# Performance work log

Hardware: AMD Instinct MI355X
Metric: run time of the kernel (lower is better)

The kernel has to match this reference:

```python
import jax, jax.numpy as jnp
import numpy as np

B, F_IN, GRID, D, C = 32768, 64, 8, 16, 10
N = GRID * GRID          # 64 nodes
HID = N * D              # 1024
ATOMS = 2
LN_EPS = 1e-5
EPS = 1e-8


def _layernorm(h):
    mu = h.mean(-1, keepdims=True)
    var = h.var(-1, keepdims=True)
    return (h - mu) / jnp.sqrt(var + LN_EPS)


def _regulator(sig, w1, b1, g, be, w2, b2):
    # Linear -> LayerNorm -> Tanh -> Linear -> Sigmoid
    h = jnp.tanh(_layernorm(sig @ w1.T + b1) * g + be)
    return jax.nn.sigmoid(h @ w2.T + b2)


def _reg_params(key, in_dim):
    k = jax.random.split(key, 4)
    return (jax.random.normal(k[0], (16, in_dim)) * 0.3,
            jax.random.normal(k[1], (16,)) * 0.1,
            jnp.ones((16,)), jnp.zeros((16,)),
            jax.random.normal(k[2], (3, 16)) * 0.3,
            jax.random.normal(k[3], (3,)) * 0.1)


def setup_inputs() -> dict:
    key = jax.random.key(0)
    ks = jax.random.split(key, 16)
    # 2D grid 4-neighbour adjacency mask (constant)
    mask = np.zeros((N, N), np.float32)
    for i in range(N):
        r, c = divmod(i, GRID)
        if r > 0: mask[i, i - GRID] = 1
        if r < GRID - 1: mask[i, i + GRID] = 1
        if c > 0: mask[i, i - 1] = 1
        if c < GRID - 1: mask[i, i + 1] = 1
    pr = _reg_params(ks[10], 3)
    cr = _reg_params(ks[11], 3)
    sr = _reg_params(ks[12], 3)
    scr = _reg_params(ks[13], 2)
    inp = {
        "x": jax.random.normal(ks[0], (B, F_IN)),
        "W_embed": jax.random.normal(ks[1], (HID, F_IN)) * 0.1,
        "b_embed": jnp.zeros((HID,)),
        "adj_weights": jax.random.normal(ks[2], (N, N)) * 0.1,
        "adj_mask": jnp.asarray(mask),
        "V_slow": jax.random.normal(ks[3], (D, D)) * 0.1,
        "W_slow": jax.random.normal(ks[4], (D, D)) * 0.1,
        "gate_w": jax.random.normal(ks[5], (1, D)) * 0.3,
        "gate_b": jnp.zeros((1,)),
        "W_fast": jax.random.normal(ks[6], (D, D)) * 0.05,  # buffer, eval mode (no Hebbian update)
        "basis": jax.random.normal(ks[7], (ATOMS, D)) * 0.5,
        "Wq": jax.random.normal(ks[8], (D, D)) * 0.2,
        "sc_w1": jax.random.normal(ks[9], (8, HID)) * 0.05,
        "sc_w2": jax.random.normal(ks[14], (4, 8)) * 0.3,
        "W_read": jax.random.normal(ks[15], (C, HID)) * 0.05,
        "b_read": jnp.zeros((C,)),
    }
    for pre, p in (("pr", pr), ("cr", cr), ("sr", sr), ("scr", scr)):
        for nm, v in zip(("w1", "b1", "g", "be", "w2", "b2"), p):
            inp[pre + "_" + nm] = v
    return inp


def reference(x, W_embed, b_embed, adj_weights, adj_mask,
              pr_w1, pr_b1, pr_g, pr_be, pr_w2, pr_b2,
              V_slow, W_slow, gate_w, gate_b, W_fast,
              cr_w1, cr_b1, cr_g, cr_be, cr_w2, cr_b2,
              basis, Wq,
              sr_w1, sr_b1, sr_g, sr_be, sr_w2, sr_b2,
              sc_w1, sc_w2,
              scr_w1, scr_b1, scr_g, scr_be, scr_w2, scr_b2,
              W_read, b_read):
    Bx = x.shape[0]
    x_embed = (x @ W_embed.T + b_embed).reshape(Bx, N, D)

    # --- AutoregulatedPlasticity adjacency ---
    sig = jnp.stack([jnp.var(x, ddof=1), jnp.abs(x_embed).mean(),
                     jnp.linalg.norm(adj_weights)])[None]
    pl = _regulator(sig, pr_w1, pr_b1, pr_g, pr_be, pr_w2, pr_b2)[0]
    adj = jax.nn.sigmoid(adj_weights * pl[0]) * adj_mask
    adj = adj / jnp.clip(adj.sum(1, keepdims=True), 1e-6, None)
    x_agg = jnp.einsum('nm,bmd->bnd', adj, x_embed)

    # --- AutoregulatedContinuum (eval: W_fast fixed) ---
    xf = x_agg.reshape(-1, D)           # [B*N, D]
    v = xf @ V_slow.T
    sig = jnp.stack([jnp.var(xf, ddof=1), jnp.abs(v).mean(),
                     jnp.linalg.norm(W_slow)])[None]
    ctrl = _regulator(sig, cr_w1, cr_b1, cr_g, cr_be, cr_w2, cr_b2)[0]
    gate = jax.nn.sigmoid(v @ gate_w.T + gate_b) * ctrl[0]   # [B*N, 1]
    fast_out = xf @ W_fast.T
    x_proc = (gate * (v + fast_out * ctrl[2])).reshape(Bx, N, D)

    # --- AutoregulatedSymbiotic, applied per node (vmapped over node axis) ---
    ortho = jnp.linalg.norm(basis @ basis.T - jnp.eye(ATOMS))
    scale = D ** 0.5 + EPS

    def sym_one(xn):  # xn: [B, D]
        w = jax.nn.softmax((xn @ Wq.T) @ basis.T / scale, axis=-1)  # [B, ATOMS]
        ent = -(w * jnp.log(w + EPS)).sum(-1).mean()
        sig_n = jnp.stack([jnp.var(xn, ddof=1), ent, ortho])[None]
        infl = _regulator(sig_n, sr_w1, sr_b1, sr_g, sr_be, sr_w2, sr_b2)[0, 0]
        return (1.0 - infl) * xn + infl * (w @ basis), ent

    refined, ents = jax.vmap(sym_one)(x_proc.transpose(1, 0, 2))  # [N,B,D]
    x_proc = refined.transpose(1, 0, 2)
    entropy = ents[-1]  # torch loop keeps the last node's entropy

    x_flat = x_proc.reshape(Bx, HID)
    logits = x_flat @ W_read.T + b_read

    # --- AutoregulatedSupConHead (entropy.item() -> detached scalar) ---
    sigc = jnp.stack([jnp.var(x_flat, ddof=1),
                      jax.lax.stop_gradient(entropy)])[None]
    gain = _regulator(sigc, scr_w1, scr_b1, scr_g, scr_be, scr_w2, scr_b2)[0, 0]
    proj = (jax.nn.relu(x_flat @ sc_w1.T) @ sc_w2.T) * gain
    return logits, proj, entropy, ortho
```

## Files before the change

kernel.cpp:

```cpp
#include <hip/hip_runtime.h>

typedef unsigned short u16;
typedef unsigned long long u64;
typedef __attribute__((ext_vector_type(8))) short short8;
typedef __attribute__((ext_vector_type(4))) float f32x4;

#define MFMA16(a,b,c) __builtin_amdgcn_mfma_f32_16x16x32_bf16(a,b,c,0,0,0)

#define B_SZ   32768
#define NNODE  64
#define NB_PAIR (B_SZ*NNODE)
#define OUT_PROJ   327680
#define OUT_ENT    458752
#define OUT_ORTHO  458753

#define OFF_SCAL   ((size_t)0)
#define OFF_ADJ    ((size_t)512)
#define OFF_BEFF   (OFF_ADJ  + 8192u)
#define OFF_WEFF   (OFF_BEFF + 4096u)
#define OFF_WCAT   (OFF_WEFF + 131072u)
#define OFF_S1     (OFF_WCAT + 65536u)
#define OFF_S2     (OFF_S1   + 12288u)
#define OFF_S3     (OFF_S2   + 12288u)
#define OFF_S4     (OFF_S3   + 2048u*192u*4u)
#define OFF_H      (OFF_S4   + 8192u)
#define OFF_W01    (OFF_H    + (size_t)B_SZ*8u*4u)
#define OFF_CAN    (OFF_W01  + (size_t)NB_PAIR*4u)

#define CAN_X      0u
#define CAN_WEMB   2097152u
#define CAN_WREAD  (CAN_WEMB + 65536u)
#define CAN_SCW1   (CAN_WREAD + 10240u)
#define CAN_SMALL  (CAN_SCW1 + 8192u)
#define CAN_TOTAL  (CAN_SMALL + 11008u)
#define OFF_BEX    (((OFF_CAN + (size_t)CAN_TOTAL*2u) + 63u) & ~(size_t)63u)
#define OFF_WET    (OFF_BEX + 48u*16u*2u)
#define OFF_VW     (OFF_WET + 131072u)
#define OFF_VB     (OFF_VW  + 131072u)
#define OFF_WC     (OFF_VB  + 4096u)
#define OFF_SW     (OFF_WC  + 131072u)
#define OFF_BC2    (OFF_SW  + 24576u)
#define OFF_SB     (OFF_BC2 + 4096u)
#define OFF_DR     (OFF_SB  + 1024u)
#define WS_NEEDED  (OFF_DR  + 192u*8u)

__device__ __forceinline__ float bf2f(u16 u){
    unsigned v = ((unsigned)u) << 16;
    return __builtin_bit_cast(float, v);
}
__device__ __forceinline__ u16 f2bf(float f){
    unsigned u = __builtin_bit_cast(unsigned, f);
    u += 0x7FFFu + ((u >> 16) & 1u);
    return (u16)(u >> 16);
}
__device__ __forceinline__ float sigm(float x){ return 1.f/(1.f + expf(-x)); }
__device__ __forceinline__ u16 conv_one(const void* src, int i, int isfp32){
    return isfp32 ? f2bf(((const float*)src)[i]) : ((const u16*)src)[i];
}
__device__ __forceinline__ void store_out(void* dout, int idx, float v, int isfp32){
    if (isfp32) ((float*)dout)[idx] = v;
    else        ((u16*)dout)[idx]   = f2bf(v);
}
__device__ __forceinline__ double blk_red(double v, double* sred, int tid){
    #pragma unroll
    for (int off = 32; off > 0; off >>= 1) v += __shfl_xor(v, off);
    if ((tid & 63) == 0) sred[tid >> 6] = v;
    __syncthreads();
    double r = sred[0] + sred[1] + sred[2] + sred[3];
    __syncthreads();
    return r;
}

__device__ void run_regulator(const u16* w1, const u16* b1, const u16* g,
                              const u16* be, const u16* w2, const u16* b2,
                              const float* sig, int in_dim, float* out)
{
    float h[16];
    float mu = 0.f;
    for (int i = 0; i < 16; ++i){
        float a = bf2f(b1[i]);
        for (int j = 0; j < in_dim; ++j) a += sig[j]*bf2f(w1[i*in_dim + j]);
        h[i] = a; mu += a;
    }
    mu *= 0.0625f;
    float var = 0.f;
    for (int i = 0; i < 16; ++i){ float d = h[i]-mu; var += d*d; }
    var *= 0.0625f;
    float inv = 1.f / sqrtf(var + 1e-5f);
    for (int i = 0; i < 16; ++i){
        float hn = (h[i]-mu)*inv;
        h[i] = tanhf(hn*bf2f(g[i]) + bf2f(be[i]));
    }
    for (int c = 0; c < 3; ++c){
        float o = bf2f(b2[c]);
        for (int i = 0; i < 16; ++i) o += h[i]*bf2f(w2[c*16 + i]);
        out[c] = sigm(o);
    }
}

__device__ __forceinline__ int probe_isfp32(const u16* xraw, int tid, int* sred)
{
    int c = 0;
    #pragma unroll
    for (int j = 0; j < 4; ++j){
        u16 u = xraw[(tid*4 + j)*2];
        int e = (u >> 7) & 0xFF;
        if (u == 0 || (e >= 90 && e <= 140)) c++;
    }
    #pragma unroll
    for (int off = 32; off > 0; off >>= 1) c += __shfl_xor(c, off);
    if ((tid & 63) == 0) sred[tid >> 6] = c;
    __syncthreads();
    int tot = sred[0]+sred[1]+sred[2]+sred[3];
    __syncthreads();
    return tot < 614;
}

__global__ __launch_bounds__(256) void kc_big(const void* x, const void* wemb,
    const void* wread, const void* scw1, u16* can, float* scal)
{
    __shared__ int sred[4];
    int tid = threadIdx.x;
    int isfp32 = probe_isfp32((const u16*)x, tid, sred);
    if (blockIdx.x == 0 && tid == 0) scal[127] = isfp32 ? 1.0f : 0.0f;
    int gid = blockIdx.x*256 + tid, stride = gridDim.x*256;
    for (int i = gid; i < 2097152; i += stride) can[CAN_X + i]     = conv_one(x, i, isfp32);
    for (int i = gid; i < 65536;   i += stride) can[CAN_WEMB + i]  = conv_one(wemb, i, isfp32);
    for (int i = gid; i < 10240;   i += stride) can[CAN_WREAD + i] = conv_one(wread, i, isfp32);
    for (int i = gid; i < 8192;    i += stride) can[CAN_SCW1 + i]  = conv_one(scw1, i, isfp32);
}

struct SmallTab { const void* src[36]; int cnt[36]; int off[36]; };
__global__ __launch_bounds__(256) void kc_small(SmallTab t, u16* can, const float* scal)
{
    int isfp32 = scal[127] != 0.f;
    int gid = blockIdx.x*256 + threadIdx.x, stride = gridDim.x*256;
    for (int e = 0; e < 36; ++e){
        const void* s = t.src[e];
        u16* d = can + t.off[e];
        int n = t.cnt[e];
        for (int i = gid; i < n; i += stride) d[i] = conv_one(s, i, isfp32);
    }
}

__global__ __launch_bounds__(256) void k0_wcat(const u16* wread, const u16* scw1,
    const u16* wemb, const u16* vslow, const u16* gatew, u16* wcat, u16* wembT, u16* bex)
{
    int b = blockIdx.x, tid = threadIdx.x;
    if (b < 128){
        int idx = b*256 + tid;
        int row = idx >> 10, k = idx & 1023;
        u16 v = 0;
        if (row < 10)      v = wread[row*1024 + k];
        else if (row < 18) v = scw1[(row-10)*1024 + k];
        wcat[idx] = v;
    } else if (b < 384){
        int idx = (b-128)*256 + tid;
        int m = idx >> 10, jj = idx & 1023;
        wembT[jj*64 + m] = wemb[m*1024 + jj];
    } else {
        if (tid < 16){
            float a = 0.f;
            for (int i = 0; i < 16; ++i) a += bf2f(gatew[i])*bf2f(vslow[i*16+tid]);
            bex[32*16+tid] = f2bf(a);
        }
    }
}

__global__ __launch_bounds__(256) void k1_embed(const u16* x, const u16* wemb,
                                                const u16* bemb, float* s1)
{
    __shared__ float red[12];
    int tid = threadIdx.x, wave = tid>>6, lane = tid&63;
    int m = lane&15, quad = lane>>4;
    int cg = blockIdx.x & 31, rc = blockIdx.x >> 5;
    int col0 = cg*32 + m, col1 = col0 + 16;
    short8 b00 = *(const short8*)(wemb + col0*64 + quad*8);
    short8 b01 = *(const short8*)(wemb + col0*64 + quad*8 + 32);
    short8 b10 = *(const short8*)(wemb + col1*64 + quad*8);
    short8 b11 = *(const short8*)(wemb + col1*64 + quad*8 + 32);
    float bias0 = bf2f(bemb[col0]), bias1 = bf2f(bemb[col1]);
    float sx = 0.f, sxx = 0.f, sabs = 0.f;
    const u16* xbase = x + (size_t)(rc*1024 + wave*256 + m)*64 + quad*8;
    #pragma unroll 4
    for (int it = 0; it < 16; ++it){
        const u16* xr = xbase + (size_t)it*16*64;
        short8 a0 = *(const short8*)xr;
        short8 a1 = *(const short8*)(xr + 32);
        if (cg == 0){
            #pragma unroll
            for (int j = 0; j < 8; ++j){
                float f0 = bf2f((u16)a0[j]); sx += f0; sxx += f0*f0;
                float f1 = bf2f((u16)a1[j]); sx += f1; sxx += f1*f1;
            }
        }
        f32x4 zc = {0.f,0.f,0.f,0.f};
        f32x4 c0 = MFMA16(a0, b00, zc);
        c0 = MFMA16(a1, b01, c0);
        f32x4 c1 = MFMA16(a0, b10, zc);
        c1 = MFMA16(a1, b11, c1);
        #pragma unroll
        for (int r = 0; r < 4; ++r)
            sabs += fabsf(c0[r]+bias0) + fabsf(c1[r]+bias1);
    }
    #pragma unroll
    for (int off = 32; off > 0; off >>= 1){
        sx   += __shfl_xor(sx, off);
        sxx  += __shfl_xor(sxx, off);
        sabs += __shfl_xor(sabs, off);
    }
    if (lane == 0){ red[wave*3] = sx; red[wave*3+1] = sxx; red[wave*3+2] = sabs; }
    __syncthreads();
    if (tid == 0){
        for (int k = 0; k < 3; ++k)
            s1[blockIdx.x*3 + k] = red[k] + red[3+k] + red[6+k] + red[9+k];
    }
}

__global__ __launch_bounds__(256) void k2_adj(const u16* adjw, const u16* adjm, const u16* bemb,
    const u16* w1, const u16* b1, const u16* g, const u16* be, const u16* w2, const u16* b2,
    const float* s1, float* scal, u16* adjb, float* beff)
{
    __shared__ double sred[4];
    __shared__ float raw[4096];
    __shared__ float rowsum[64];
    __shared__ float bembs[1024];
    __shared__ float pl0s;
    int tid = threadIdx.x;
    for (int i = tid; i < 1024; i += 256) bembs[i] = bf2f(bemb[i]);
    double s=0, ss=0, sa=0;
    for (int i = tid; i < 1024; i += 256){
        s += (double)s1[i*3]; ss += (double)s1[i*3+1]; sa += (double)s1[i*3+2];
    }
    double nq = 0;
    for (int i = tid; i < 4096; i += 256){ float f = bf2f(adjw[i]); nq += (double)(f*f); }
    double S  = blk_red(s,  sred, tid);
    double SS = blk_red(ss, sred, tid);
    double SA = blk_red(sa, sred, tid);
    double NQ = blk_red(nq, sred, tid);
    if (tid == 0){
        double nx = 2097152.0;
        float sg[3];
        sg[0] = (float)((SS - S*S/nx)/(nx - 1.0));
        sg[1] = (float)(SA / 33554432.0);
        sg[2] = sqrtf((float)NQ);
        float o[3];
        run_regulator(w1,b1,g,be,w2,b2, sg, 3, o);
        scal[0] = o[0]; pl0s = o[0];
    }
    __syncthreads();
    float pl0 = pl0s;
    for (int i = tid; i < 4096; i += 256)
        raw[i] = sigm(bf2f(adjw[i])*pl0) * bf2f(adjm[i]);
    __syncthreads();
    if (tid < 64){
        float r = 0.f;
        for (int mc = 0; mc < 64; ++mc) r += raw[tid*64 + mc];
        rowsum[tid] = fmaxf(r, 1e-6f);
    }
    __syncthreads();
    for (int i = tid; i < 4096; i += 256) adjb[i] = f2bf(raw[i] / rowsum[i>>6]);
    for (int o = tid; o < 1024; o += 256){
        int n = o >> 4, d = o & 15;
        float a = 0.f;
        for (int m = 0; m < 64; ++m) a += raw[n*64+m]*bembs[m*16+d];
        beff[o] = a / rowsum[n];
    }
}

__global__ __launch_bounds__(256) void k2b_mfma(const u16* adjb, const u16* wembT, u16* weff)
{
    int tid = threadIdx.x, wave = tid>>6, lane = tid&63;
    int m = lane&15, quad = lane>>4;
    const u16* ar = adjb + (wave*16 + m)*64 + quad*8;
    short8 a0 = *(const short8*)ar;
    short8 a1 = *(const short8*)(ar + 32);
    int col = blockIdx.x*16 + m;
    const u16* br = wembT + col*64 + quad*8;
    short8 b0 = *(const short8*)br;
    short8 b1 = *(const short8*)(br + 32);
    f32x4 acc = {0.f,0.f,0.f,0.f};
    acc = MFMA16(a0, b0, acc);
    acc = MFMA16(a1, b1, acc);
    #pragma unroll
    for (int r = 0; r < 4; ++r)
        weff[(size_t)(wave*16 + quad*4 + r)*1024 + blockIdx.x*16 + m] = f2bf(acc[r]);
}

__global__ __launch_bounds__(256) void kvw(const u16* vslow, const u16* weff, const float* beff,
                                           u16* vw, float* vbias)
{
    __shared__ float Vs[256];
    int tid = threadIdx.x, b = blockIdx.x;
    Vs[tid] = bf2f(vslow[tid]);
    __syncthreads();
    if (b < 256){
        int idx = b*256 + tid;
        int j = idx >> 6, kf = idx & 63;
        int n = j >> 4, i = j & 15;
        float a = 0.f;
        #pragma unroll
        for (int d = 0; d < 16; ++d) a += Vs[i*16+d]*bf2f(weff[(size_t)(n*16+d)*64 + kf]);
        vw[(size_t)j*64 + kf] = f2bf(a);
    } else {
        int o = (b-256)*256 + tid;
        int n = o >> 4, i = o & 15;
        float a = 0.f;
        #pragma unroll
        for (int d = 0; d < 16; ++d) a += Vs[i*16+d]*beff[n*16+d];
        vbias[o] = a;
    }
}

__global__ __launch_bounds__(256) void k3_stats(const u16* x, const u16* weff, const float* beff,
                                                const u16* vw, const float* vbias, float* s2)
{
    __shared__ float red[12];
    int tid = threadIdx.x, wave = tid>>6, lane = tid&63;
    int m = lane&15, quad = lane>>4;
    int cg = blockIdx.x & 31, rc = blockIdx.x >> 5;
    int col0 = cg*32 + m, col1 = col0 + 16;
    short8 b00 = *(const short8*)(weff + (size_t)col0*64 + quad*8);
    short8 b01 = *(const short8*)(weff + (size_t)col0*64 + quad*8 + 32);
    short8 b10 = *(const short8*)(weff + (size_t)col1*64 + quad*8);
    short8 b11 = *(const short8*)(weff + (size_t)col1*64 + quad*8 + 32);
    short8 v00 = *(const short8*)(vw + (size_t)col0*64 + quad*8);
    short8 v01 = *(const short8*)(vw + (size_t)col0*64 + quad*8 + 32);
    short8 v10 = *(const short8*)(vw + (size_t)col1*64 + quad*8);
    short8 v11 = *(const short8*)(vw + (size_t)col1*64 + quad*8 + 32);
    float be0 = beff[col0], be1 = beff[col1];
    float vb0 = vbias[col0], vb1 = vbias[col1];
    float psum=0.f, pssq=0.f, pabsv=0.f;
    const u16* xbase = x + (size_t)(rc*1024 + wave*256 + m)*64 + quad*8;
    #pragma unroll 4
    for (int it = 0; it < 16; ++it){
        const u16* xr = xbase + (size_t)it*16*64;
        short8 a0 = *(const short8*)xr;
        short8 a1 = *(const short8*)(xr + 32);
        f32x4 zc = {0.f,0.f,0.f,0.f};
        f32x4 c0 = MFMA16(a0, b00, zc);
        c0 = MFMA16(a1, b01, c0);
        f32x4 c1 = MFMA16(a0, b10, zc);
        c1 = MFMA16(a1, b11, c1);
        f32x4 w0 = MFMA16(a0, v00, zc);
        w0 = MFMA16(a1, v01, w0);
        f32x4 w1 = MFMA16(a0, v10, zc);
        w1 = MFMA16(a1, v11, w1);
        #pragma unroll
        for (int r = 0; r < 4; ++r){
            float f0 = c0[r] + be0, f1 = c1[r] + be1;
            psum += f0 + f1; pssq += f0*f0 + f1*f1;
            pabsv += fabsf(w0[r] + vb0) + fabsf(w1[r] + vb1);
        }
    }
    #pragma unroll
    for (int off = 32; off > 0; off >>= 1){
        psum  += __shfl_xor(psum, off);
        pssq  += __shfl_xor(pssq, off);
        pabsv += __shfl_xor(pabsv, off);
    }
    if (lane == 0){ red[wave*3] = psum; red[wave*3+1] = pssq; red[wave*3+2] = pabsv; }
    __syncthreads();
    if (tid == 0){
        for (int k = 0; k < 3; ++k)
            s2[blockIdx.x*3 + k] = red[k] + red[3+k] + red[6+k] + red[9+k];
    }
}

__global__ __launch_bounds__(256) void k3b_ctrl(const u16* wslow,
    const u16* vslow, const u16* wfast, const u16* wq, const u16* basis,
    const u16* w1, const u16* b1, const u16* g, const u16* be, const u16* w2, const u16* b2,
    const float* s2, float* scal, u16* bex)
{
    __shared__ double sred[4];
    __shared__ float ctrl2s;
    int tid = threadIdx.x;
    double s=0, ss=0, sv=0;
    for (int i = tid; i < 1024; i += 256){
        s += (double)s2[i*3]; ss += (double)s2[i*3+1]; sv += (double)s2[i*3+2];
    }
    float wf = bf2f(wslow[tid]);
    double nq = (double)(wf*wf);
    double S  = blk_red(s,  sred, tid);
    double SS = blk_red(ss, sred, tid);
    double SV = blk_red(sv, sred, tid);
    double NQ = blk_red(nq, sred, tid);
    if (tid == 0){
        double M = 33554432.0;
        float sg[3];
        sg[0] = (float)((SS - S*S/M)/(M - 1.0));
        sg[1] = (float)(SV / M);
        sg[2] = sqrtf((float)NQ);
        float o[3];
        run_regulator(w1,b1,g,be,w2,b2, sg, 3, o);
        scal[1] = o[0]; scal[2] = o[2];
        ctrl2s = o[2];
    }
    __syncthreads();
    float ctrl2 = ctrl2s;
    if (tid < 64){
        #pragma unroll
        for (int j = 0; j < 4; ++j){
            int idx = tid*4 + j;
            int d = idx >> 4, k = idx & 15;
            bex[(16+d)*16+k] = f2bf(bf2f(vslow[idx]) + ctrl2*bf2f(wfast[idx]));
        }
    } else if (tid < 96){
        int a = (tid-64) >> 4, k = (tid-64) & 15;
        float e = 0.f;
        for (int d = 0; d < 16; ++d){
            float bq = 0.f;
            for (int j = 0; j < 16; ++j) bq += bf2f(basis[a*16+j])*bf2f(wq[j*16+d]);
            e += bq*(bf2f(vslow[d*16+k]) + ctrl2*bf2f(wfast[d*16+k]));
        }
        bex[(33+a)*16+k] = f2bf(0.25f*e);
    }
}

__global__ __launch_bounds__(256) void kbw(const u16* bex, const u16* weff, const float* beff,
                                           const u16* gateb, u16* wc, u16* sw,
                                           float* bc, float* sb)
{
    __shared__ float BcL[256], gvL[16], e0L[16], e1L[16];
    int tid = threadIdx.x;
    if (tid < 256) BcL[tid] = bf2f(bex[(16 + (tid>>4))*16 + (tid&15)]);
    if (tid < 16){
        gvL[tid] = bf2f(bex[32*16+tid]);
        e0L[tid] = bf2f(bex[33*16+tid]);
        e1L[tid] = bf2f(bex[34*16+tid]);
    }
    __syncthreads();
    int id = blockIdx.x*256 + tid;
    if (id < 65536){
        int col = id >> 6, k = id & 63;
        int n = col >> 4, d = col & 15;
        float a = 0.f;
        #pragma unroll
        for (int dd = 0; dd < 16; ++dd)
            a += BcL[d*16+dd]*bf2f(weff[(size_t)(n*16+dd)*64 + k]);
        wc[(size_t)col*64 + k] = f2bf(a);
    } else if (id < 77824){
        int j2 = id - 65536;
        int scol = j2 >> 6, k = j2 & 63;
        int n = scol/3, j = scol - n*3;
        const float* sr = (j==0) ? gvL : (j==1) ? e0L : e1L;
        float a = 0.f;
        #pragma unroll
        for (int dd = 0; dd < 16; ++dd)
            a += sr[dd]*bf2f(weff[(size_t)(n*16+dd)*64 + k]);
        sw[(size_t)scol*64 + k] = f2bf(a);
    } else if (id < 78848){
        int col = id - 77824;
        int n = col >> 4, d = col & 15;
        float a = 0.f;
        #pragma unroll
        for (int dd = 0; dd < 16; ++dd) a += BcL[d*16+dd]*beff[n*16+dd];
        bc[col] = a;
    } else if (id < 79040){
        int s = id - 78848;
        int n = s/3, j = s - n*3;
        const float* sr = (j==0) ? gvL : (j==1) ? e0L : e1L;
        float a = 0.f;
        #pragma unroll
        for (int dd = 0; dd < 16; ++dd) a += sr[dd]*beff[n*16+dd];
        if (j == 0) a += bf2f(gateb[0]);
        sb[s] = a;
    }
}

#define SCP 193
__global__ __launch_bounds__(256) void k4_stats(const u16* x, const u16* wc, const u16* sw,
    const float* bc, const float* sb, const float* scal, unsigned* wpack, float* s3)
{
    __shared__ float sc[16*SCP];
    __shared__ float gt[1024];
    __shared__ float entp[256];
    __shared__ float snode[128];
    int tid = threadIdx.x, wave = tid>>6, lane = tid&63;
    int m = lane&15, quad = lane>>4;
    int row0 = blockIdx.x*16;
    const u16* xr = x + (row0 + m)*64 + quad*8;
    short8 a0 = *(const short8*)xr;
    short8 a1 = *(const short8*)(xr + 32);
    float ctrl0 = scal[1];
    #pragma unroll
    for (int tt = 0; tt < 3; ++tt){
        int ct = wave*3 + tt;
        int scol = ct*16 + m;
        const u16* br = sw + (size_t)scol*64 + quad*8;
        short8 b0 = *(const short8*)br;
        short8 b1 = *(const short8*)(br + 32);
        f32x4 zc = {0.f,0.f,0.f,0.f};
        f32x4 c = MFMA16(a0, b0, zc);
        c = MFMA16(a1, b1, c);
        float sbv = sb[scol];
        #pragma unroll
        for (int r = 0; r < 4; ++r)
            sc[(quad*4+r)*SCP + scol] = c[r] + sbv;
    }
    __syncthreads();
    {
        int n = tid & 63, rgrp = tid >> 6;
        float ent = 0.f;
        #pragma unroll
        for (int rr = 0; rr < 4; ++rr){
            int row = rgrp*4 + rr;
            float gd  = sc[row*SCP + 3*n];
            float e0d = sc[row*SCP + 3*n + 1];
            float e1d = sc[row*SCP + 3*n + 2];
            float gate = ctrl0 / (1.f + __expf(-gd));
            float l0 = gate*e0d, l1 = gate*e1d;
            float w1v = 1.f/(1.f + __expf(l0 - l1));
            float w0v = 1.f - w1v;
            ent += -(w0v*__logf(w0v + 1e-8f) + w1v*__logf(w1v + 1e-8f));
            gt[row*64 + n] = gate;
            wpack[(size_t)(row0 + row)*64 + n] =
                ((unsigned)f2bf(w0v) << 16) | (unsigned)f2bf(gate);
        }
        entp[tid] = ent;
    }
    __syncthreads();
    #pragma unroll
    for (int tt = 0; tt < 16; ++tt){
        int n = wave*16 + tt;
        int col = n*16 + m;
        const u16* br = wc + (size_t)col*64 + quad*8;
        short8 b0 = *(const short8*)br;
        short8 b1 = *(const short8*)(br + 32);
        f32x4 zc = {0.f,0.f,0.f,0.f};
        f32x4 c = MFMA16(a0, b0, zc);
        c = MFMA16(a1, b1, c);
        float bcv = bc[col];
        float ps = 0.f, pq = 0.f;
        #pragma unroll
        for (int r = 0; r < 4; ++r){
            float gate = gt[(quad*4+r)*64 + n];
            float xp = gate*(c[r] + bcv);
            ps += xp; pq += xp*xp;
        }
        #pragma unroll
        for (int off = 32; off > 0; off >>= 1){
            ps += __shfl_xor(ps, off);
            pq += __shfl_xor(pq, off);
        }
        if (lane == 0){ snode[n] = ps; snode[64+n] = pq; }
    }
    __syncthreads();
    if (tid < 192){
        float v;
        if (tid < 128) v = snode[tid];
        else { int n = tid-128; v = entp[n]+entp[64+n]+entp[128+n]+entp[192+n]; }
        s3[(size_t)blockIdx.x*192 + tid] = v;
    }
}

__global__ __launch_bounds__(256) void k5a_red(const float* s3, double* dred)
{
    __shared__ double sred[4];
    int tid = threadIdx.x, col = blockIdx.x;
    double a = 0;
    for (int i = tid; i < 2048; i += 256) a += (double)s3[(size_t)i*192 + col];
    #pragma unroll
    for (int off = 32; off > 0; off >>= 1) a += __shfl_xor(a, off);
    if ((tid & 63) == 0) sred[tid >> 6] = a;
    __syncthreads();
    if (tid == 0) dred[col] = sred[0]+sred[1]+sred[2]+sred[3];
}

__global__ __launch_bounds__(64) void k5b_infl(const u16* basis,
    const u16* w1, const u16* b1, const u16* g, const u16* be, const u16* w2, const u16* b2,
    const double* dred, float* scal, void* dout)
{
    int n = threadIdx.x;
    int isfp32 = scal[127] != 0.f;
    double sum = dred[n], ssq = dred[64+n], ent = dred[128+n];
    double Mn = 524288.0;
    float varn = (float)((ssq - sum*sum/Mn)/(Mn - 1.0));
    float entm = (float)(ent / 32768.0);
    float b0[16], b1v[16];
    for (int d = 0; d < 16; ++d){ b0[d] = bf2f(basis[d]); b1v[d] = bf2f(basis[16+d]); }
    float g00=0.f, g01=0.f, g11=0.f;
    for (int d = 0; d < 16; ++d){ g00 += b0[d]*b0[d]; g01 += b0[d]*b1v[d]; g11 += b1v[d]*b1v[d]; }
    float ortho = sqrtf((g00-1.f)*(g00-1.f) + 2.f*g01*g01 + (g11-1.f)*(g11-1.f));
    float sg[3] = {varn, entm, ortho};
    float o[3];
    run_regulator(w1,b1,g,be,w2,b2, sg, 3, o);
    scal[4+n] = o[0];
    if (n == 63){ scal[68] = entm;  store_out(dout, OUT_ENT,   entm,  isfp32); }
    if (n == 0) { scal[69] = ortho; store_out(dout, OUT_ORTHO, ortho, isfp32); }
}

#define XSP 136
__global__ __launch_bounds__(256, 2) void k6_read(const u16* x, const unsigned* wpack,
    const u16* wc, const float* bc, const u16* wcat,
    const u16* basis, const u16* bread, const float* scal,
    void* dout, float* hbuf, float* s4)
{
    __shared__ unsigned gwP[64*65];
    __shared__ __align__(16) u16 xs[4*16*XSP];
    __shared__ float infl_s[64], b0s[16], b1s[16], brd[16];
    __shared__ float red[8];
    int tid = threadIdx.x;
    int isfp32 = scal[127] != 0.f;
    for (int i = tid; i < 4096; i += 256)
        gwP[(i >> 6)*65 + (i & 63)] = wpack[(size_t)blockIdx.x*4096 + i];
    if (tid < 64) infl_s[tid] = scal[4+tid];
    if (tid < 16){
        b0s[tid] = bf2f(basis[tid]);
        b1s[tid] = bf2f(basis[16+tid]);
        brd[tid] = (tid < 10) ? bf2f(bread[tid]) : 0.f;
    }
    __syncthreads();
    int wave = tid>>6, lane = tid&63;
    int m = lane&15, quad = lane>>4;
    int row = blockIdx.x*64 + wave*16 + m;
    const u16* xr = x + (size_t)row*64 + quad*8;
    short8 a0 = *(const short8*)xr;
    short8 a1 = *(const short8*)(xr + 32);
    float b0d[4], b1d[4];
    #pragma unroll
    for (int r = 0; r < 4; ++r){ b0d[r] = b0s[quad*4+r]; b1d[r] = b1s[quad*4+r]; }
    u16* xsw = xs + wave*16*XSP;
    const unsigned* gwrow = gwP + (wave*16 + m)*65;
    f32x4 acc0 = {0.f,0.f,0.f,0.f}, acc1 = {0.f,0.f,0.f,0.f};
    float psum = 0.f, pssq = 0.f;
    for (int c8 = 0; c8 < 8; ++c8){
        f32x4 cT[8], bc4[8];
        unsigned gv[8];
        float fiv[8];
        #pragma unroll
        for (int t = 0; t < 8; ++t){
            int n = c8*8 + t;
            int col = n*16 + m;
            const u16* br = wc + (size_t)col*64 + quad*8;
            short8 wf0 = *(const short8*)br;
            short8 wf1 = *(const short8*)(br + 32);
            f32x4 zc = {0.f,0.f,0.f,0.f};
            f32x4 cc = MFMA16(wf0, a0, zc);
            cc = MFMA16(wf1, a1, cc);
            cT[t] = cc;
            bc4[t] = *(const f32x4*)(bc + n*16 + quad*4);
            gv[t]  = gwrow[n];
            fiv[t] = infl_s[n];
        }
        #pragma unroll
        for (int t = 0; t < 8; ++t){
            float gate = bf2f((u16)(gv[t] & 0xFFFFu));
            float w0v  = bf2f((u16)(gv[t] >> 16));
            float fi = fiv[t], om = 1.f - fi;
            u64 pk = 0;
            #pragma unroll
            for (int r = 0; r < 4; ++r){
                float xp = gate*(cT[t][r] + bc4[t][r]);
                float bb = w0v*b0d[r] + (1.f - w0v)*b1d[r];
                float xf = om*xp + fi*bb;
                psum += xf; pssq += xf*xf;
                pk |= ((u64)f2bf(xf)) << (r*16);
            }
            *(u64*)(xsw + m*XSP + t*16 + quad*4) = pk;
        }
        #pragma unroll
        for (int kk = 0; kk < 4; ++kk){
            short8 af = *(const short8*)(xsw + m*XSP + kk*32 + quad*8);
            short8 bb0 = *(const short8*)(wcat + m*1024      + c8*128 + kk*32 + quad*8);
            short8 bb1 = *(const short8*)(wcat + (16+m)*1024 + c8*128 + kk*32 + quad*8);
            acc0 = MFMA16(af, bb0, acc0);
            acc1 = MFMA16(af, bb1, acc1);
        }
    }
    int rowbase = blockIdx.x*64 + wave*16 + quad*4;
    #pragma unroll
    for (int r = 0; r < 4; ++r){
        int rowg = rowbase + r;
        if (m < 10) store_out(dout, rowg*10 + m, acc0[r] + brd[m], isfp32);
        else        hbuf[rowg*8 + (m-10)] = fmaxf(acc0[r], 0.f);
        if (m < 2)  hbuf[rowg*8 + 6 + m]  = fmaxf(acc1[r], 0.f);
    }
    #pragma unroll
    for (int off = 32; off > 0; off >>= 1){
        psum += __shfl_xor(psum, off);
        pssq += __shfl_xor(pssq, off);
    }
    if (lane == 0){ red[wave] = psum; red[4+wave] = pssq; }
    __syncthreads();
    if (tid == 0){
        s4[blockIdx.x*2]   = red[0]+red[1]+red[2]+red[3];
        s4[blockIdx.x*2+1] = red[4]+red[5]+red[6]+red[7];
    }
}

__global__ __launch_bounds__(256) void k8_proj(const float* hbuf, const u16* scw2,
    const u16* w1, const u16* b1, const u16* g, const u16* be, const u16* w2, const u16* b2,
    const float* s4, const float* scal, void* dout)
{
    __shared__ double sred[4];
    __shared__ float w2s[32];
    __shared__ float gains;
    int tid = threadIdx.x;
    int isfp32 = scal[127] != 0.f;
    if (tid < 32) w2s[tid] = bf2f(scw2[tid]);
    double s=0, ss=0;
    for (int i = tid; i < 512; i += 256){ s += (double)s4[i*2]; ss += (double)s4[i*2+1]; }
    double S  = blk_red(s,  sred, tid);
    double SS = blk_red(ss, sred, tid);
    if (tid == 0){
        double M = 33554432.0;
        float sg[2];
        sg[0] = (float)((SS - S*S/M)/(M - 1.0));
        sg[1] = scal[68];
        float o[3];
        run_regulator(w1,b1,g,be,w2,b2, sg, 2, o);
        gains = o[0];
    }
    __syncthreads();
    float gain = gains;
    int b = blockIdx.x*256 + tid;
    const float* h = hbuf + (size_t)b*8;
    float hv[8];
    #pragma unroll
    for (int k = 0; k < 8; ++k) hv[k] = h[k];
    #pragma unroll
    for (int i = 0; i < 4; ++i){
        float o = 0.f;
        #pragma unroll
        for (int k = 0; k < 8; ++k) o += hv[k]*w2s[i*8+k];
        store_out(dout, OUT_PROJ + b*4 + i, o*gain, isfp32);
    }
}

extern "C" void kernel_launch(void* const* d_in, const int* in_sizes, int n_in,
                              void* d_out, int out_size, void* d_ws, size_t ws_size,
                              hipStream_t stream)
{
    if (ws_size < WS_NEEDED) return;

    char* ws = (char*)d_ws;
    float* scal  = (float*)(ws + OFF_SCAL);
    u16*   adjb  = (u16*)  (ws + OFF_ADJ);
    float* beff  = (float*)(ws + OFF_BEFF);
    u16*   weff  = (u16*)  (ws + OFF_WEFF);
    u16*   wcat  = (u16*)  (ws + OFF_WCAT);
    float* s1    = (float*)(ws + OFF_S1);
    float* s2    = (float*)(ws + OFF_S2);
    float* s3    = (float*)(ws + OFF_S3);
    float* s4    = (float*)(ws + OFF_S4);
    float* hbuf  = (float*)(ws + OFF_H);
    unsigned* wpack = (unsigned*)(ws + OFF_W01);
    u16*   can   = (u16*)  (ws + OFF_CAN);
    u16*   bex   = (u16*)  (ws + OFF_BEX);
    u16*   wembT = (u16*)  (ws + OFF_WET);
    u16*   vw    = (u16*)  (ws + OFF_VW);
    float* vbias = (float*)(ws + OFF_VB);
    u16*   wc    = (u16*)  (ws + OFF_WC);
    u16*   sw    = (u16*)  (ws + OFF_SW);
    float* bc    = (float*)(ws + OFF_BC2);
    float* sb    = (float*)(ws + OFF_SB);
    double* dred = (double*)(ws + OFF_DR);

    static const int sidx[36] = {2,3,4,5,6,7,8,9,10,11,13,15,
        16,17,18,19,20,21, 22,23,24,25,26,27, 28,29,30,31,32,33, 34,35,36,37,38,39};
    static const int scnt[36] = {1024,4096,4096,256,256,16,1,256,32,256,32,10,
        48,16,16,16,48,3, 48,16,16,16,48,3, 48,16,16,16,48,3, 32,16,16,16,48,3};
    SmallTab t;
    const u16* canp[40];
    {
        int off = (int)CAN_SMALL;
        for (int j = 0; j < 36; ++j){
            t.src[j] = d_in[sidx[j]];
            t.cnt[j] = scnt[j];
            t.off[j] = off;
            canp[sidx[j]] = can + off;
            off += (scnt[j] + 7) & ~7;
        }
    }
    canp[0]  = can + CAN_X;
    canp[1]  = can + CAN_WEMB;
    canp[12] = can + CAN_SCW1;
    canp[14] = can + CAN_WREAD;

    const u16* pr_[6]; const u16* cr_[6]; const u16* sr_[6]; const u16* sc_[6];
    for (int i = 0; i < 6; ++i){
        pr_[i] = canp[16+i]; cr_[i] = canp[22+i];
        sr_[i] = canp[28+i]; sc_[i] = canp[34+i];
    }

    kc_big  <<<1024,256, 0, stream>>>(d_in[0], d_in[1], d_in[14], d_in[12], can, scal);
    kc_small<<<16,  256, 0, stream>>>(t, can, scal);
    k0_wcat <<<385, 256, 0, stream>>>(canp[14], canp[12], canp[1], canp[5], canp[7],
                 wcat, wembT, bex);
    k1_embed<<<1024,256, 0, stream>>>(canp[0], canp[1], canp[2], s1);
    k2_adj  <<<1,   256, 0, stream>>>(canp[3], canp[4], canp[2],
                 pr_[0],pr_[1],pr_[2],pr_[3],pr_[4],pr_[5], s1, scal, adjb, beff);
    k2b_mfma<<<64,  256, 0, stream>>>(adjb, wembT, weff);
    kvw     <<<260, 256, 0, stream>>>(canp[5], weff, beff, vw, vbias);
    k3_stats<<<1024,256, 0, stream>>>(canp[0], weff, beff, vw, vbias, s2);
    k3b_ctrl<<<1,   256, 0, stream>>>(canp[6], canp[5], canp[9], canp[11], canp[10],
                 cr_[0],cr_[1],cr_[2],cr_[3],cr_[4],cr_[5], s2, scal, bex);
    kbw     <<<312, 256, 0, stream>>>(bex, weff, beff, canp[8], wc, sw, bc, sb);
    k4_stats<<<2048,256, 0, stream>>>(canp[0], wc, sw, bc, sb, scal, wpack, s3);
    k5a_red <<<192, 256, 0, stream>>>(s3, dred);
    k5b_infl<<<1,   64,  0, stream>>>(canp[10],
                 sr_[0],sr_[1],sr_[2],sr_[3],sr_[4],sr_[5], dred, scal, d_out);
    k6_read <<<512, 256, 0, stream>>>(canp[0], wpack, wc, bc, wcat, canp[10], canp[15],
                 scal, d_out, hbuf, s4);
    k8_proj <<<128, 256, 0, stream>>>(hbuf, canp[13],
                 sc_[0],sc_[1],sc_[2],sc_[3],sc_[4],sc_[5], s4, scal, d_out);
}
```

Before: 346.0 us.

## Merge small conversion kernels and resize k6_read to 128-thread blocks

Fuses kc_small and k0_wcat into one kernel, kc_rest. Because of the fusion, the bex computation now converts the raw gate/vslow inputs itself instead of waiting for converted copies. k6_read moves from 512 blocks of 256 threads to 1024 blocks of 128 threads, each handling 32 rows, and raises launch bounds to 4 blocks per SM. It also stages bc into shared memory, splits the 8-tile inner loop into two halves of 4 to reduce register pressure, and folds the blend algebra into fewer multiplies. The goal is to save a launch and raise occupancy in k6_read, at the cost of twice as many partial sums for k8_proj to reduce and more wpack/bc staging per row.

After: 344.7 us. About the same (-0.4%).

```diff
diff --git a/kernel.cpp b/kernel.cpp
--- a/kernel.cpp
+++ b/kernel.cpp
@@ -131,37 +131,37 @@
 }
 
 struct SmallTab { const void* src[36]; int cnt[36]; int off[36]; };
-__global__ __launch_bounds__(256) void kc_small(SmallTab t, u16* can, const float* scal)
-{
+__global__ __launch_bounds__(256) void kc_rest(SmallTab t,
+    const void* vslow_raw, const void* gatew_raw,
+    const u16* wread, const u16* scw1, const u16* wemb,
+    u16* can, const float* scal, u16* wcat, u16* wembT, u16* bex)
+{
+    int b = blockIdx.x, tid = threadIdx.x;
     int isfp32 = scal[127] != 0.f;
-    int gid = blockIdx.x*256 + threadIdx.x, stride = gridDim.x*256;
-    for (int e = 0; e < 36; ++e){
-        const void* s = t.src[e];
-        u16* d = can + t.off[e];
-        int n = t.cnt[e];
-        for (int i = gid; i < n; i += stride) d[i] = conv_one(s, i, isfp32);
-    }
-}
-
-__global__ __launch_bounds__(256) void k0_wcat(const u16* wread, const u16* scw1,
-    const u16* wemb, const u16* vslow, const u16* gatew, u16* wcat, u16* wembT, u16* bex)
-{
-    int b = blockIdx.x, tid = threadIdx.x;
-    if (b < 128){
-        int idx = b*256 + tid;
+    if (b < 16){
+        int gid = b*256 + tid, stride = 16*256;
+        for (int e = 0; e < 36; ++e){
+            const void* s = t.src[e];
+            u16* d = can + t.off[e];
+            int n = t.cnt[e];
+            for (int i = gid; i < n; i += stride) d[i] = conv_one(s, i, isfp32);
+        }
+    } else if (b < 144){
+        int idx = (b-16)*256 + tid;
         int row = idx >> 10, k = idx & 1023;
         u16 v = 0;
         if (row < 10)      v = wread[row*1024 + k];
         else if (row < 18) v = scw1[(row-10)*1024 + k];
         wcat[idx] = v;
-    } else if (b < 384){
-        int idx = (b-128)*256 + tid;
+    } else if (b < 400){
+        int idx = (b-144)*256 + tid;
         int m = idx >> 10, jj = idx & 1023;
         wembT[jj*64 + m] = wemb[m*1024 + jj];
     } else {
         if (tid < 16){
             float a = 0.f;
-            for (int i = 0; i < 16; ++i) a += bf2f(gatew[i])*bf2f(vslow[i*16+tid]);
+            for (int i = 0; i < 16; ++i)
+                a += bf2f(conv_one(gatew_raw, i, isfp32))*bf2f(conv_one(vslow_raw, i*16+tid, isfp32));
             bex[32*16+tid] = f2bf(a);
         }
     }
@@ -590,20 +590,22 @@
     if (n == 0) { scal[69] = ortho; store_out(dout, OUT_ORTHO, ortho, isfp32); }
 }
 
-#define XSP 136
-__global__ __launch_bounds__(256, 2) void k6_read(const u16* x, const unsigned* wpack,
+#define XSP 132
+__global__ __launch_bounds__(128, 4) void k6_read(const u16* x, const unsigned* wpack,
     const u16* wc, const float* bc, const u16* wcat,
     const u16* basis, const u16* bread, const float* scal,
     void* dout, float* hbuf, float* s4)
 {
-    __shared__ unsigned gwP[64*65];
-    __shared__ __align__(16) u16 xs[4*16*XSP];
+    __shared__ unsigned gwP[32*65];
+    __shared__ __align__(16) u16 xs[2*16*XSP];
+    __shared__ float bc_s[1024];
     __shared__ float infl_s[64], b0s[16], b1s[16], brd[16];
-    __shared__ float red[8];
+    __shared__ float red[4];
     int tid = threadIdx.x;
     int isfp32 = scal[127] != 0.f;
-    for (int i = tid; i < 4096; i += 256)
-        gwP[(i >> 6)*65 + (i & 63)] = wpack[(size_t)blockIdx.x*4096 + i];
+    for (int i = tid; i < 2048; i += 128)
+        gwP[(i >> 6)*65 + (i & 63)] = wpack[(size_t)blockIdx.x*2048 + i];
+    for (int i = tid; i < 1024; i += 128) bc_s[i] = bc[i];
     if (tid < 64) infl_s[tid] = scal[4+tid];
     if (tid < 16){
         b0s[tid] = bf2f(basis[tid]);
@@ -613,7 +615,7 @@
     __syncthreads();
     int wave = tid>>6, lane = tid&63;
     int m = lane&15, quad = lane>>4;
-    int row = blockIdx.x*64 + wave*16 + m;
+    int row = blockIdx.x*32 + wave*16 + m;
     const u16* xr = x + (size_t)row*64 + quad*8;
     short8 a0 = *(const short8*)xr;
     short8 a1 = *(const short8*)(xr + 32);
@@ -625,39 +627,45 @@
     f32x4 acc0 = {0.f,0.f,0.f,0.f}, acc1 = {0.f,0.f,0.f,0.f};
     float psum = 0.f, pssq = 0.f;
     for (int c8 = 0; c8 < 8; ++c8){
-        f32x4 cT[8], bc4[8];
-        unsigned gv[8];
-        float fiv[8];
-        #pragma unroll
-        for (int t = 0; t < 8; ++t){
-            int n = c8*8 + t;
-            int col = n*16 + m;
-            const u16* br = wc + (size_t)col*64 + quad*8;
-            short8 wf0 = *(const short8*)br;
-            short8 wf1 = *(const short8*)(br + 32);
-            f32x4 zc = {0.f,0.f,0.f,0.f};
-            f32x4 cc = MFMA16(wf0, a0, zc);
-            cc = MFMA16(wf1, a1, cc);
-            cT[t] = cc;
-            bc4[t] = *(const f32x4*)(bc + n*16 + quad*4);
-            gv[t]  = gwrow[n];
-            fiv[t] = infl_s[n];
-        }
-        #pragma unroll
-        for (int t = 0; t < 8; ++t){
-            float gate = bf2f((u16)(gv[t] & 0xFFFFu));
-            float w0v  = bf2f((u16)(gv[t] >> 16));
-            float fi = fiv[t], om = 1.f - fi;
-            u64 pk = 0;
+        #pragma unroll
+        for (int hf = 0; hf < 2; ++hf){
+            f32x4 cT[4], bc4[4];
+            unsigned gv[4];
+            float fiv[4];
             #pragma unroll
-            for (int r = 0; r < 4; ++r){
-                float xp = gate*(cT[t][r] + bc4[t][r]);
-                float bb = w0v*b0d[r] + (1.f - w0v)*b1d[r];
-                float xf = om*xp + fi*bb;
-                psum += xf; pssq += xf*xf;
-                pk |= ((u64)f2bf(xf)) << (r*16);
+            for (int j = 0; j < 4; ++j){
+                int n = c8*8 + hf*4 + j;
+                int col = n*16 + m;
+                const u16* br = wc + (size_t)col*64 + quad*8;
+                short8 wf0 = *(const short8*)br;
+                short8 wf1 = *(const short8*)(br + 32);
+                f32x4 zc = {0.f,0.f,0.f,0.f};
+                f32x4 cc = MFMA16(wf0, a0, zc);
+                cc = MFMA16(wf1, a1, cc);
+                cT[j] = cc;
+                bc4[j] = *(const f32x4*)(bc_s + n*16 + quad*4);
+                gv[j]  = gwrow[n];
+                fiv[j] = infl_s[n];
             }
-            *(u64*)(xsw + m*XSP + t*16 + quad*4) = pk;
+            #pragma unroll
+            for (int j = 0; j < 4; ++j){
+                int t = hf*4 + j;
+                float gate = bf2f((u16)(gv[j] & 0xFFFFu));
+                float w0v  = bf2f((u16)(gv[j] >> 16));
+                float fi = fiv[j];
+                float A   = (1.f - fi)*gate;
+                float fw0 = fi*w0v;
+                float fw1 = fi - fw0;
+                u64 pk = 0;
+                #pragma unroll
+                for (int r = 0; r < 4; ++r){
+                    float base = fw0*b0d[r] + fw1*b1d[r];
+                    float v = A*(cT[j][r] + bc4[j][r]) + base;
+                    psum += v; pssq += v*v;
+                    pk |= ((u64)f2bf(v)) << (r*16);
+                }
+                *(u64*)(xsw + m*XSP + t*16 + quad*4) = pk;
+            }
         }
         #pragma unroll
         for (int kk = 0; kk < 4; ++kk){
@@ -668,7 +676,7 @@
             acc1 = MFMA16(af, bb1, acc1);
         }
     }
-    int rowbase = blockIdx.x*64 + wave*16 + quad*4;
+    int rowbase = blockIdx.x*32 + wave*16 + quad*4;
     #pragma unroll
     for (int r = 0; r < 4; ++r){
         int rowg = rowbase + r;
@@ -681,11 +689,11 @@
         psum += __shfl_xor(psum, off);
         pssq += __shfl_xor(pssq, off);
     }
-    if (lane == 0){ red[wave] = psum; red[4+wave] = pssq; }
+    if (lane == 0){ red[wave] = psum; red[2+wave] = pssq; }
     __syncthreads();
     if (tid == 0){
-        s4[blockIdx.x*2]   = red[0]+red[1]+red[2]+red[3];
-        s4[blockIdx.x*2+1] = red[4]+red[5]+red[6]+red[7];
+        s4[blockIdx.x*2]   = red[0]+red[1];
+        s4[blockIdx.x*2+1] = red[2]+red[3];
     }
 }
 
@@ -700,7 +708,7 @@
     int isfp32 = scal[127] != 0.f;
     if (tid < 32) w2s[tid] = bf2f(scw2[tid]);
     double s=0, ss=0;
-    for (int i = tid; i < 512; i += 256){ s += (double)s4[i*2]; ss += (double)s4[i*2+1]; }
+    for (int i = tid; i < 1024; i += 256){ s += (double)s4[i*2]; ss += (double)s4[i*2+1]; }
     double S  = blk_red(s,  sred, tid);
     double SS = blk_red(ss, sred, tid);
     if (tid == 0){
@@ -785,9 +793,8 @@
     }
 
     kc_big  <<<1024,256, 0, stream>>>(d_in[0], d_in[1], d_in[14], d_in[12], can, scal);
-    kc_small<<<16,  256, 0, stream>>>(t, can, scal);
-    k0_wcat <<<385, 256, 0, stream>>>(canp[14], canp[12], canp[1], canp[5], canp[7],
-                 wcat, wembT, bex);
+    kc_rest <<<401, 256, 0, stream>>>(t, d_in[5], d_in[7], canp[14], canp[12], canp[1],
+                 can, scal, wcat, wembT, bex);
     k1_embed<<<1024,256, 0, stream>>>(canp[0], canp[1], canp[2], s1);
     k2_adj  <<<1,   256, 0, stream>>>(canp[3], canp[4], canp[2],
                  pr_[0],pr_[1],pr_[2],pr_[3],pr_[4],pr_[5], s1, scal, adjb, beff);
@@ -801,7 +808,7 @@
     k5a_red <<<192, 256, 0, stream>>>(s3, dred);
     k5b_infl<<<1,   64,  0, stream>>>(canp[10],
                  sr_[0],sr_[1],sr_[2],sr_[3],sr_[4],sr_[5], dred, scal, d_out);
-    k6_read <<<512, 256, 0, stream>>>(canp[0], wpack, wc, bc, wcat, canp[10], canp[15],
+    k6_read <<<1024,128, 0, stream>>>(canp[0], wpack, wc, bc, wcat, canp[10], canp[15],
                  scal, d_out, hbuf, s4);
     k8_proj <<<128, 256, 0, stream>>>(hbuf, canp[13],
                  sc_[0],sc_[1],sc_[2],sc_[3],sc_[4],sc_[5], s4, scal, d_out);
```
